# Kernel tuning notes

Measured on AMD Instinct MI355X. Metric: run time of the kernel, lower is better.

The kernel has to match this reference:

```python
import jax, jax.numpy as jnp
import numpy as np

B, N, D = 16, 2048, 256  # batch (pairs*2), num_keypoints, descriptor_dim


def setup_inputs() -> dict:
    key = jax.random.key(0)
    k1, k2, k3, k4 = jax.random.split(key, 4)
    descriptors = jax.random.normal(k1, (B, N, D), dtype=jnp.float32)
    mask = jax.random.randint(k2, (B, N), 0, 2, dtype=jnp.int32)
    proj_w = jax.random.normal(k3, (D, D), dtype=jnp.float32) * 0.02
    proj_b = jnp.zeros((D,), dtype=jnp.float32)
    match_w = jax.random.normal(k4, (1, D), dtype=jnp.float32) * 0.02
    match_b = jnp.zeros((1,), dtype=jnp.float32)
    return {"descriptors": descriptors, "mask": mask, "proj_w": proj_w,
            "proj_b": proj_b, "match_w": match_w, "match_b": match_b}


def reference(descriptors, mask, proj_w, proj_b, match_w, match_b):
    batch, n, d = descriptors.shape
    pairs = batch // 2
    # final projection + temperature scaling
    m_desc = (descriptors @ proj_w.T + proj_b) / jnp.asarray(d, descriptors.dtype) ** 0.25
    m_desc = m_desc.reshape(pairs, 2, n, d)
    # similarity: [pairs, n0, n1]
    similarity = jnp.einsum('bnd,bmd->bnm', m_desc[:, 0], m_desc[:, 1])
    mask_p = mask.reshape(pairs, 2, n)
    pair_mask = mask_p[:, 0][:, :, None] * mask_p[:, 1][:, None, :]
    neg_min = jnp.finfo(similarity.dtype).min
    similarity = jnp.where(pair_mask == 0, neg_min, similarity)
    # matchability logits: [B, n, 1] -> split per pair
    matchability = (descriptors @ match_w.T + match_b).reshape(pairs, 2, n)
    m0 = matchability[:, 0]  # [pairs, n]
    m1 = matchability[:, 1]  # [pairs, n]
    certainties = jax.nn.log_sigmoid(m0)[:, :, None] + jax.nn.log_sigmoid(m1)[:, None, :]
    scores0 = jax.nn.log_softmax(similarity, axis=2)
    scores1 = jax.nn.log_softmax(similarity, axis=1)
    inner = scores0 + scores1 + certainties
    scores = jnp.zeros((pairs, n + 1, n + 1), dtype=similarity.dtype)
    scores = scores.at[:, :n, :n].set(inner)
    scores = scores.at[:, :-1, -1].set(jax.nn.log_sigmoid(-m0))
    scores = scores.at[:, -1, :-1].set(jax.nn.log_sigmoid(-m1))
    return scores
```

## Files before the change

### kernel.cpp

```cpp
#include <hip/hip_runtime.h>
#include <math.h>

typedef unsigned short u16;
typedef __attribute__((ext_vector_type(8))) short bf16x8;
typedef __attribute__((ext_vector_type(4))) float f32x4;

#define BN 16
#define N 2048
#define D 256
#define PAIRS 8
#define NO 2049
#define NEGMIN  -3.40282347e38f
#define MASKVAL -3.0e38f
#define LDA 72

#define WS_LS0   0
#define WS_LS1   (1*PAIRS*N)
#define WS_LSN0  (2*PAIRS*N)
#define WS_LSN1  (3*PAIRS*N)
#define WS_RMAX  (4*PAIRS*N)
#define WS_RLSE  (5*PAIRS*N)
#define WS_CMAX  (6*PAIRS*N)
#define WS_CLSE  (7*PAIRS*N)
#define WS_RPM   (8*PAIRS*N)
#define WS_RPS   (WS_RPM + PAIRS*16*N)
#define WS_CPM   (WS_RPS + PAIRS*16*N)
#define WS_CPS   (WS_CPM + PAIRS*16*N)
#define WS_F_COUNT (WS_CPS + PAIRS*16*N)

__device__ __forceinline__ float b2f(u16 u) {
    return __uint_as_float(((unsigned)u) << 16);
}
__device__ __forceinline__ u16 f2b(float f) {
    unsigned x = __float_as_uint(f);
    x += 0x7FFFu + ((x >> 16) & 1u);
    return (u16)(x >> 16);
}
__device__ __forceinline__ unsigned pk2(float a, float b) {
    return (unsigned)f2b(a) | ((unsigned)f2b(b) << 16);
}
__device__ __forceinline__ float logsig(float x) {
    return fminf(x, 0.f) - log1pf(expf(-fabsf(x)));
}
__device__ __forceinline__ void online1(float& m, float& s, float x) {
    float nm = fmaxf(m, x);
    float e = __expf(fminf(m, x) - nm);
    s = (x > m) ? s * e + 1.f : s + e;
    m = nm;
}
__device__ __forceinline__ void onmerge(float& m, float& s, float om, float os) {
    float nm = fmaxf(m, om);
    s = s * __expf(m - nm) + os * __expf(om - nm);
    m = nm;
}

__global__ __launch_bounds__(256) void k_proj_mfma(const float* __restrict__ A,
                                                   const float* __restrict__ W,
                                                   const float* __restrict__ bias,
                                                   const float* __restrict__ mw,
                                                   const float* __restrict__ mb,
                                                   u16* __restrict__ mdesc,
                                                   float* __restrict__ wsf) {
    __shared__ u16 As[128 * LDA];
    __shared__ u16 Bs[128 * LDA];
    int r0 = blockIdx.x * 128, c0 = blockIdx.y * 128;
    int tid = threadIdx.x;
    int w = tid >> 6, lane = tid & 63;
    int ln = lane & 15, q = lane >> 4;
    int wr0 = (w >> 1) * 64, wc0 = (w & 1) * 64;
    f32x4 zero = {0.f, 0.f, 0.f, 0.f};
    f32x4 acc[4][4];
    #pragma unroll
    for (int a = 0; a < 4; ++a)
        #pragma unroll
        for (int b = 0; b < 4; ++b) acc[a][b] = zero;
    float mdot[4] = {0.f, 0.f, 0.f, 0.f};
    int domatch = (blockIdx.y == 0);

    for (int kb = 0; kb < D; kb += 64) {
        __syncthreads();
        #pragma unroll
        for (int t = 0; t < 4; ++t) {
            int c = t * 256 + tid;
            int row = c >> 3, part = c & 7;
            const float* ap = A + (size_t)(r0 + row) * D + kb + part * 8;
            float4 f0 = *(const float4*)ap;
            float4 f1 = *(const float4*)(ap + 4);
            uint4 va;
            va.x = pk2(f0.x, f0.y); va.y = pk2(f0.z, f0.w);
            va.z = pk2(f1.x, f1.y); va.w = pk2(f1.z, f1.w);
            *(uint4*)&As[row * LDA + part * 8] = va;
            if (domatch) {
                float4 w0 = *(const float4*)(mw + kb + part * 8);
                float4 w1 = *(const float4*)(mw + kb + part * 8 + 4);
                mdot[t] += f0.x*w0.x + f0.y*w0.y + f0.z*w0.z + f0.w*w0.w
                         + f1.x*w1.x + f1.y*w1.y + f1.z*w1.z + f1.w*w1.w;
            }
            const float* bp = W + (size_t)(c0 + row) * D + kb + part * 8;
            float4 g0 = *(const float4*)bp;
            float4 g1 = *(const float4*)(bp + 4);
            uint4 vb;
            vb.x = pk2(g0.x, g0.y); vb.y = pk2(g0.z, g0.w);
            vb.z = pk2(g1.x, g1.y); vb.w = pk2(g1.z, g1.w);
            *(uint4*)&Bs[row * LDA + part * 8] = vb;
        }
        __syncthreads();
        #pragma unroll
        for (int kk = 0; kk < 64; kk += 32) {
            bf16x8 af[4], bf[4];
            #pragma unroll
            for (int ri = 0; ri < 4; ++ri)
                af[ri] = *(const bf16x8*)&As[(wr0 + ri*16 + ln) * LDA + kk + q*8];
            #pragma unroll
            for (int ci = 0; ci < 4; ++ci)
                bf[ci] = *(const bf16x8*)&Bs[(wc0 + ci*16 + ln) * LDA + kk + q*8];
            #pragma unroll
            for (int ri = 0; ri < 4; ++ri)
                #pragma unroll
                for (int ci = 0; ci < 4; ++ci)
                    acc[ri][ci] = __builtin_amdgcn_mfma_f32_16x16x32_bf16(af[ri], bf[ci], acc[ri][ci], 0, 0, 0);
        }
    }
    if (domatch) {
        #pragma unroll
        for (int t = 0; t < 4; ++t) {
            float s = mdot[t];
            s += __shfl_xor(s, 1, 64);
            s += __shfl_xor(s, 2, 64);
            s += __shfl_xor(s, 4, 64);
            if ((tid & 7) == 0) {
                int row_g = r0 + t * 32 + (tid >> 3);
                float m = s + mb[0];
                int b = row_g >> 11;
                int i = row_g & (N - 1);
                int pp = b >> 1, sid = b & 1;
                float ls = logsig(m), lsn = logsig(-m);
                if (sid == 0) { wsf[WS_LS0 + pp*N + i] = ls; wsf[WS_LSN0 + pp*N + i] = lsn; }
                else          { wsf[WS_LS1 + pp*N + i] = ls; wsf[WS_LSN1 + pp*N + i] = lsn; }
            }
        }
    }
    #pragma unroll
    for (int ri = 0; ri < 4; ++ri) {
        #pragma unroll
        for (int reg = 0; reg < 4; ++reg) {
            int row = r0 + wr0 + ri*16 + q*4 + reg;
            #pragma unroll
            for (int ci = 0; ci < 4; ++ci) {
                int col = c0 + wc0 + ci*16 + ln;
                float v = (acc[ri][ci][reg] + bias[col]) * 0.25f;
                mdesc[(size_t)row * D + col] = f2b(v);
            }
        }
    }
}

__global__ __launch_bounds__(256) void k_sim_mfma(const u16* __restrict__ mdesc,
                                                  const int* __restrict__ mask,
                                                  u16* __restrict__ out,
                                                  float* __restrict__ wsf) {
    __shared__ u16 As[128 * LDA];
    __shared__ u16 Bs[128 * LDA];
    __shared__ float rpm[128][2], rps[128][2];
    __shared__ float cpm[128][2], cps[128][2];
    int p = blockIdx.z;
    const u16* A  = mdesc + (size_t)(2*p) * N * D;
    const u16* Bm = mdesc + (size_t)(2*p + 1) * N * D;
    int r0 = blockIdx.x * 128, c0 = blockIdx.y * 128;
    int tid = threadIdx.x;
    int w = tid >> 6, lane = tid & 63;
    int ln = lane & 15, q = lane >> 4;
    int wr0 = (w >> 1) * 64, wc0 = (w & 1) * 64;
    f32x4 zero = {0.f, 0.f, 0.f, 0.f};
    f32x4 acc[4][4];
    #pragma unroll
    for (int a = 0; a < 4; ++a)
        #pragma unroll
        for (int b = 0; b < 4; ++b) acc[a][b] = zero;

    for (int kb = 0; kb < D; kb += 64) {
        __syncthreads();
        #pragma unroll
        for (int t = 0; t < 4; ++t) {
            int c = t * 256 + tid;
            int row = c >> 3, part = c & 7;
            uint4 va = *(const uint4*)(A  + (size_t)(r0 + row) * D + kb + part * 8);
            *(uint4*)&As[row * LDA + part * 8] = va;
            uint4 vb = *(const uint4*)(Bm + (size_t)(c0 + row) * D + kb + part * 8);
            *(uint4*)&Bs[row * LDA + part * 8] = vb;
        }
        __syncthreads();
        #pragma unroll
        for (int kk = 0; kk < 64; kk += 32) {
            bf16x8 af[4], bf[4];
            #pragma unroll
            for (int ri = 0; ri < 4; ++ri)
                af[ri] = *(const bf16x8*)&As[(wr0 + ri*16 + ln) * LDA + kk + q*8];
            #pragma unroll
            for (int ci = 0; ci < 4; ++ci)
                bf[ci] = *(const bf16x8*)&Bs[(wc0 + ci*16 + ln) * LDA + kk + q*8];
            #pragma unroll
            for (int ri = 0; ri < 4; ++ri)
                #pragma unroll
                for (int ci = 0; ci < 4; ++ci)
                    acc[ri][ci] = __builtin_amdgcn_mfma_f32_16x16x32_bf16(af[ri], bf[ci], acc[ri][ci], 0, 0, 0);
        }
    }
    const int* m0 = mask + (size_t)(2*p) * N;
    const int* m1 = mask + (size_t)(2*p + 1) * N;
    u16* outp = out + (size_t)p * NO * NO;
    int mcol[4];
    #pragma unroll
    for (int ci = 0; ci < 4; ++ci) mcol[ci] = m1[c0 + wc0 + ci*16 + ln];
    #pragma unroll
    for (int ri = 0; ri < 4; ++ri) {
        #pragma unroll
        for (int reg = 0; reg < 4; ++reg) {
            int row = r0 + wr0 + ri*16 + q*4 + reg;
            int mr = m0[row];
            size_t base = (size_t)row * NO + c0 + wc0 + ln;
            #pragma unroll
            for (int ci = 0; ci < 4; ++ci) {
                float v = (mr && mcol[ci]) ? acc[ri][ci][reg] : MASKVAL;
                acc[ri][ci][reg] = v;
                outp[base + ci*16] = f2b(v);
            }
        }
    }
    #pragma unroll
    for (int ri = 0; ri < 4; ++ri) {
        #pragma unroll
        for (int reg = 0; reg < 4; ++reg) {
            float m = acc[ri][0][reg], s = 1.f;
            online1(m, s, acc[ri][1][reg]);
            online1(m, s, acc[ri][2][reg]);
            online1(m, s, acc[ri][3][reg]);
            #pragma unroll
            for (int off = 1; off <= 8; off <<= 1) {
                float om = __shfl_xor(m, off, 64);
                float os = __shfl_xor(s, off, 64);
                onmerge(m, s, om, os);
            }
            if (ln == 0) {
                int rl = wr0 + ri*16 + q*4 + reg;
                rpm[rl][w & 1] = m; rps[rl][w & 1] = s;
            }
        }
    }
    #pragma unroll
    for (int ci = 0; ci < 4; ++ci) {
        float m = acc[0][ci][0], s = 1.f;
        #pragma unroll
        for (int ri = 0; ri < 4; ++ri)
            #pragma unroll
            for (int reg = 0; reg < 4; ++reg)
                if (!(ri == 0 && reg == 0)) online1(m, s, acc[ri][ci][reg]);
        #pragma unroll
        for (int off = 16; off <= 32; off <<= 1) {
            float om = __shfl_xor(m, off, 64);
            float os = __shfl_xor(s, off, 64);
            onmerge(m, s, om, os);
        }
        if (q == 0) {
            int cl = wc0 + ci*16 + ln;
            cpm[cl][w >> 1] = m; cps[cl][w >> 1] = s;
        }
    }
    __syncthreads();
    if (tid < 128) {
        float m = rpm[tid][0], s = rps[tid][0];
        onmerge(m, s, rpm[tid][1], rps[tid][1]);
        size_t o = (size_t)(p * 16 + blockIdx.y) * N + r0 + tid;
        wsf[WS_RPM + o] = m; wsf[WS_RPS + o] = s;
    } else {
        int c = tid - 128;
        float m = cpm[c][0], s = cps[c][0];
        onmerge(m, s, cpm[c][1], cps[c][1]);
        size_t o = (size_t)(p * 16 + blockIdx.x) * N + c0 + c;
        wsf[WS_CPM + o] = m; wsf[WS_CPS + o] = s;
    }
}

__global__ __launch_bounds__(256) void k_red(float* __restrict__ wsf) {
    int i = blockIdx.x * 256 + threadIdx.x;
    int p = blockIdx.y;
    if (blockIdx.z == 0) {
        float m = wsf[WS_RPM + (size_t)(p*16) * N + i];
        float s = wsf[WS_RPS + (size_t)(p*16) * N + i];
        for (int cb = 1; cb < 16; ++cb)
            onmerge(m, s, wsf[WS_RPM + (size_t)(p*16 + cb) * N + i],
                          wsf[WS_RPS + (size_t)(p*16 + cb) * N + i]);
        wsf[WS_RMAX + p * N + i] = m;
        wsf[WS_RLSE + p * N + i] = logf(s);
    } else {
        float m = wsf[WS_CPM + (size_t)(p*16) * N + i];
        float s = wsf[WS_CPS + (size_t)(p*16) * N + i];
        for (int rb = 1; rb < 16; ++rb)
            onmerge(m, s, wsf[WS_CPM + (size_t)(p*16 + rb) * N + i],
                          wsf[WS_CPS + (size_t)(p*16 + rb) * N + i]);
        wsf[WS_CMAX + p * N + i] = m;
        wsf[WS_CLSE + p * N + i] = logf(s);
    }
}

__global__ __launch_bounds__(256) void k_final(u16* __restrict__ out,
                                               const float* __restrict__ wsf) {
    int i = blockIdx.x, p = blockIdx.y;
    int tid = threadIdx.x;
    size_t B0 = ((size_t)p * NO + i) * NO;
    unsigned* up = (unsigned*)out;
    int head = (int)(B0 & 1);
    size_t U0 = (B0 + head) >> 1;
    if (i < N) {
        float rm  = wsf[WS_RMAX + p*N + i];
        float rl  = wsf[WS_RLSE + p*N + i];
        float l0  = wsf[WS_LS0  + p*N + i];
        float ln0 = wsf[WS_LSN0 + p*N + i];
        for (int k = tid; k < 1024; k += 256) {
            unsigned v = up[U0 + k];
            int j0 = 2*k + head;
            float o0, o1;
            {
                float x = b2f((u16)v);
                float a = (x - rm) - rl;
                float b = (x - wsf[WS_CMAX + p*N + j0]) - wsf[WS_CLSE + p*N + j0];
                o0 = fmaxf(fmaxf(a + b, MASKVAL) + (l0 + wsf[WS_LS1 + p*N + j0]), MASKVAL);
            }
            int j1 = j0 + 1;
            if (j1 < N) {
                float x = b2f((u16)(v >> 16));
                float a = (x - rm) - rl;
                float b = (x - wsf[WS_CMAX + p*N + j1]) - wsf[WS_CLSE + p*N + j1];
                o1 = fmaxf(fmaxf(a + b, MASKVAL) + (l0 + wsf[WS_LS1 + p*N + j1]), MASKVAL);
            } else {
                o1 = ln0;
            }
            up[U0 + k] = pk2(o0, o1);
        }
        if (tid == 0) {
            if (head) {
                float x = b2f(out[B0]);
                float a = (x - rm) - rl;
                float b = (x - wsf[WS_CMAX + p*N]) - wsf[WS_CLSE + p*N];
                out[B0] = f2b(fmaxf(fmaxf(a + b, MASKVAL) + (l0 + wsf[WS_LS1 + p*N]), MASKVAL));
            } else {
                out[B0 + N] = f2b(ln0);
            }
        }
    } else {
        for (int k = tid; k < 1024; k += 256) {
            int j0 = 2*k + head;
            float o0 = (j0 < N) ? wsf[WS_LSN1 + p*N + j0] : 0.f;
            int j1 = j0 + 1;
            float o1 = (j1 < N) ? wsf[WS_LSN1 + p*N + j1] : 0.f;
            up[U0 + k] = pk2(o0, o1);
        }
        if (tid == 0) {
            if (head) out[B0] = f2b(wsf[WS_LSN1 + p*N]);
            else      out[B0 + N] = 0;
        }
    }
}

extern "C" void kernel_launch(void* const* d_in, const int* in_sizes, int n_in,
                              void* d_out, int out_size, void* d_ws, size_t ws_size,
                              hipStream_t stream) {
    const float* desc    = (const float*)d_in[0];
    const int*   mask    = (const int*)d_in[1];
    const float* proj_w  = (const float*)d_in[2];
    const float* proj_b  = (const float*)d_in[3];
    const float* match_w = (const float*)d_in[4];
    const float* match_b = (const float*)d_in[5];
    u16*   out = (u16*)d_out;
    float* wsf = (float*)d_ws;
    u16*   mdesc = (u16*)((char*)d_ws + (size_t)WS_F_COUNT * sizeof(float));

    k_proj_mfma<<<dim3(256, 2),    256, 0, stream>>>(desc, proj_w, proj_b, match_w, match_b, mdesc, wsf);
    k_sim_mfma <<<dim3(16, 16, 8), 256, 0, stream>>>(mdesc, mask, out, wsf);
    k_red      <<<dim3(8, 8, 2),   256, 0, stream>>>(wsf);
    k_final    <<<dim3(2049, 8),   256, 0, stream>>>(out, wsf);
}
```

Measured before the change: 275.3 us.

## Fuse row log-sum-exp reduction into final pass and process 8 rows per block

Moves the row-partial merge out of the reduction kernel into the final kernel, where each block merges the 16 column-block partials for its 8 rows with wave shuffles. Each block now covers 8 output rows, so the per-column statistics (column max, column LSE, log-sigmoid) are loaded once into registers and reused across all 8 rows instead of being reloaded per row. The grid shrinks from 2049 to 257 blocks per pair, and the row parity is computed as (p+i)&1. This cuts the reduction work and the redundant global loads, but the final kernel has fewer blocks and does more serial work per thread.

```diff
diff --git a/kernel.cpp b/kernel.cpp
--- a/kernel.cpp
+++ b/kernel.cpp
@@ -5,7 +5,6 @@
 typedef __attribute__((ext_vector_type(8))) short bf16x8;
 typedef __attribute__((ext_vector_type(4))) float f32x4;
 
-#define BN 16
 #define N 2048
 #define D 256
 #define PAIRS 8
@@ -284,80 +283,110 @@
 __global__ __launch_bounds__(256) void k_red(float* __restrict__ wsf) {
     int i = blockIdx.x * 256 + threadIdx.x;
     int p = blockIdx.y;
-    if (blockIdx.z == 0) {
-        float m = wsf[WS_RPM + (size_t)(p*16) * N + i];
-        float s = wsf[WS_RPS + (size_t)(p*16) * N + i];
-        for (int cb = 1; cb < 16; ++cb)
-            onmerge(m, s, wsf[WS_RPM + (size_t)(p*16 + cb) * N + i],
-                          wsf[WS_RPS + (size_t)(p*16 + cb) * N + i]);
-        wsf[WS_RMAX + p * N + i] = m;
-        wsf[WS_RLSE + p * N + i] = logf(s);
-    } else {
-        float m = wsf[WS_CPM + (size_t)(p*16) * N + i];
-        float s = wsf[WS_CPS + (size_t)(p*16) * N + i];
-        for (int rb = 1; rb < 16; ++rb)
-            onmerge(m, s, wsf[WS_CPM + (size_t)(p*16 + rb) * N + i],
-                          wsf[WS_CPS + (size_t)(p*16 + rb) * N + i]);
-        wsf[WS_CMAX + p * N + i] = m;
-        wsf[WS_CLSE + p * N + i] = logf(s);
-    }
+    float m = wsf[WS_CPM + (size_t)(p*16) * N + i];
+    float s = wsf[WS_CPS + (size_t)(p*16) * N + i];
+    for (int rb = 1; rb < 16; ++rb)
+        onmerge(m, s, wsf[WS_CPM + (size_t)(p*16 + rb) * N + i],
+                      wsf[WS_CPS + (size_t)(p*16 + rb) * N + i]);
+    wsf[WS_CMAX + p * N + i] = m;
+    wsf[WS_CLSE + p * N + i] = logf(s);
 }
 
 __global__ __launch_bounds__(256) void k_final(u16* __restrict__ out,
                                                const float* __restrict__ wsf) {
-    int i = blockIdx.x, p = blockIdx.y;
+    int strip = blockIdx.x;
+    int p = blockIdx.y;
     int tid = threadIdx.x;
-    size_t B0 = ((size_t)p * NO + i) * NO;
+    __shared__ float rm_l[8], rl_l[8], l0_l[8], ln0_l[8];
+    if (tid < 128) {
+        int r = tid >> 4, cb = tid & 15;
+        int i = strip * 8 + r;
+        if (i < N) {
+            float m = wsf[WS_RPM + (size_t)(p*16 + cb) * N + i];
+            float sv = wsf[WS_RPS + (size_t)(p*16 + cb) * N + i];
+            #pragma unroll
+            for (int off = 1; off <= 8; off <<= 1) {
+                float om = __shfl_xor(m, off, 64);
+                float os = __shfl_xor(sv, off, 64);
+                onmerge(m, sv, om, os);
+            }
+            if (cb == 0) {
+                rm_l[r]  = m;
+                rl_l[r]  = logf(sv);
+                l0_l[r]  = wsf[WS_LS0  + p*N + i];
+                ln0_l[r] = wsf[WS_LSN0 + p*N + i];
+            }
+        }
+    }
+    __syncthreads();
     unsigned* up = (unsigned*)out;
-    int head = (int)(B0 & 1);
-    size_t U0 = (B0 + head) >> 1;
-    if (i < N) {
-        float rm  = wsf[WS_RMAX + p*N + i];
-        float rl  = wsf[WS_RLSE + p*N + i];
-        float l0  = wsf[WS_LS0  + p*N + i];
-        float ln0 = wsf[WS_LSN0 + p*N + i];
-        for (int k = tid; k < 1024; k += 256) {
-            unsigned v = up[U0 + k];
-            int j0 = 2*k + head;
-            float o0, o1;
-            {
-                float x = b2f((u16)v);
-                float a = (x - rm) - rl;
-                float b = (x - wsf[WS_CMAX + p*N + j0]) - wsf[WS_CLSE + p*N + j0];
-                o0 = fmaxf(fmaxf(a + b, MASKVAL) + (l0 + wsf[WS_LS1 + p*N + j0]), MASKVAL);
-            }
-            int j1 = j0 + 1;
+    #pragma unroll
+    for (int k = 0; k < 4; ++k) {
+        int kk = k * 256 + tid;
+        int jc = 2 * kk;
+        float cm0 = wsf[WS_CMAX + p*N + jc];
+        float cl0 = wsf[WS_CLSE + p*N + jc];
+        float s10 = wsf[WS_LS1  + p*N + jc];
+        float cm1 = wsf[WS_CMAX + p*N + jc + 1];
+        float cl1 = wsf[WS_CLSE + p*N + jc + 1];
+        float s11 = wsf[WS_LS1  + p*N + jc + 1];
+        float cm2 = 0.f, cl2 = 0.f, s12 = 0.f;
+        if (jc + 2 < N) {
+            cm2 = wsf[WS_CMAX + p*N + jc + 2];
+            cl2 = wsf[WS_CLSE + p*N + jc + 2];
+            s12 = wsf[WS_LS1  + p*N + jc + 2];
+        }
+        for (int r = 0; r < 8; ++r) {
+            int i = strip * 8 + r;
+            if (i > N) break;
+            size_t B0 = ((size_t)p * NO + i) * NO;
+            int head = (p + i) & 1;
+            size_t U0 = (B0 + head) >> 1;
+            if (i == N) {
+                int j0 = 2*kk + head;
+                float o0 = (j0 < N) ? wsf[WS_LSN1 + p*N + j0] : 0.f;
+                int j1 = j0 + 1;
+                float o1 = (j1 < N) ? wsf[WS_LSN1 + p*N + j1] : 0.f;
+                up[U0 + kk] = pk2(o0, o1);
+                if (tid == 0 && k == 0) {
+                    if (head) out[B0] = f2b(wsf[WS_LSN1 + p*N]);
+                    else      out[B0 + N] = 0;
+                }
+                continue;
+            }
+            float rm = rm_l[r], rl = rl_l[r], l0 = l0_l[r], ln0 = ln0_l[r];
+            unsigned v = up[U0 + kk];
+            float cmA = head ? cm1 : cm0;
+            float clA = head ? cl1 : cl0;
+            float s1A = head ? s11 : s10;
+            float x0 = b2f((u16)v);
+            float a0 = (x0 - rm) - rl;
+            float b0 = (x0 - cmA) - clA;
+            float o0 = fmaxf(fmaxf(a0 + b0, MASKVAL) + (l0 + s1A), MASKVAL);
+            float o1;
+            int j1 = 2*kk + head + 1;
             if (j1 < N) {
-                float x = b2f((u16)(v >> 16));
-                float a = (x - rm) - rl;
-                float b = (x - wsf[WS_CMAX + p*N + j1]) - wsf[WS_CLSE + p*N + j1];
-                o1 = fmaxf(fmaxf(a + b, MASKVAL) + (l0 + wsf[WS_LS1 + p*N + j1]), MASKVAL);
+                float cmB = head ? cm2 : cm1;
+                float clB = head ? cl2 : cl1;
+                float s1B = head ? s12 : s11;
+                float x1 = b2f((u16)(v >> 16));
+                float a1 = (x1 - rm) - rl;
+                float b1 = (x1 - cmB) - clB;
+                o1 = fmaxf(fmaxf(a1 + b1, MASKVAL) + (l0 + s1B), MASKVAL);
             } else {
                 o1 = ln0;
             }
-            up[U0 + k] = pk2(o0, o1);
-        }
-        if (tid == 0) {
-            if (head) {
-                float x = b2f(out[B0]);
-                float a = (x - rm) - rl;
-                float b = (x - wsf[WS_CMAX + p*N]) - wsf[WS_CLSE + p*N];
-                out[B0] = f2b(fmaxf(fmaxf(a + b, MASKVAL) + (l0 + wsf[WS_LS1 + p*N]), MASKVAL));
-            } else {
-                out[B0 + N] = f2b(ln0);
-            }
-        }
-    } else {
-        for (int k = tid; k < 1024; k += 256) {
-            int j0 = 2*k + head;
-            float o0 = (j0 < N) ? wsf[WS_LSN1 + p*N + j0] : 0.f;
-            int j1 = j0 + 1;
-            float o1 = (j1 < N) ? wsf[WS_LSN1 + p*N + j1] : 0.f;
-            up[U0 + k] = pk2(o0, o1);
-        }
-        if (tid == 0) {
-            if (head) out[B0] = f2b(wsf[WS_LSN1 + p*N]);
-            else      out[B0 + N] = 0;
+            up[U0 + kk] = pk2(o0, o1);
+            if (tid == 0 && k == 0) {
+                if (head) {
+                    float x = b2f(out[B0]);
+                    float a = (x - rm) - rl;
+                    float b = (x - wsf[WS_CMAX + p*N]) - wsf[WS_CLSE + p*N];
+                    out[B0] = f2b(fmaxf(fmaxf(a + b, MASKVAL) + (l0 + wsf[WS_LS1 + p*N]), MASKVAL));
+                } else {
+                    out[B0 + N] = f2b(ln0);
+                }
+            }
         }
     }
 }
@@ -377,6 +406,6 @@
 
     k_proj_mfma<<<dim3(256, 2),    256, 0, stream>>>(desc, proj_w, proj_b, match_w, match_b, mdesc, wsf);
     k_sim_mfma <<<dim3(16, 16, 8), 256, 0, stream>>>(mdesc, mask, out, wsf);
-    k_red      <<<dim3(8, 8, 2),   256, 0, stream>>>(wsf);
-    k_final    <<<dim3(2049, 8),   256, 0, stream>>>(out, wsf);
-}
+    k_red      <<<dim3(8, 8),      256, 0, stream>>>(wsf);
+    k_final    <<<dim3(257, 8),    256, 0, stream>>>(out, wsf);
+}
```

Measured after the change: 255.2 us. 1.08x faster.
